# Kernel optimization log

Measured on AMD Instinct MI355X. Metric: run time of the kernel, lower is better.

Reference implementation:

```python
import jax, jax.numpy as jnp
import numpy as np

INP = 1024          # inp_size
N = 8000            # n_neurons
NE = 6400           # n_e_neurons = 0.8*N
NI = 1600           # n_i_neurons = 0.2*N
TS = 1000           # ts_sim = t_sim/dt = 1.0/0.001
PRB0, PRB1 = 200, 1000  # probe window in timesteps
DT = 0.001
TAU = 0.02
VTH = 0.5
RATE = 0.5          # rate_scale
NORM = float(PRB1 - PRB0)  # spike_p_norm


def setup_inputs() -> dict:
    key = jax.random.key(0)
    k1, k2, k3, k4, k5, k6 = jax.random.split(key, 6)
    inp = jax.random.uniform(k1, (INP,), dtype=jnp.float32)
    A = INP + N
    # Sparse random recurrent weights, faithful in structure to init_w:
    # rows [0:INP+NE] carry excitatory (positive) weights, last NI rows inhibitory (negative).
    sign = jnp.concatenate([jnp.ones(INP + NE, jnp.float32), -jnp.ones(NI, jnp.float32)])[:, None]
    mask_e = (jax.random.uniform(k2, (A, NE)) < 0.05).astype(jnp.float32)
    w_ae = sign * mask_e * jax.random.uniform(k3, (A, NE), dtype=jnp.float32) * 0.1
    mask_i = (jax.random.uniform(k4, (A, NI)) < 0.05).astype(jnp.float32)
    w_ai = sign * mask_i * jax.random.uniform(k5, (A, NI), dtype=jnp.float32) * 0.1
    # Precomputed per-timestep uniform noise (replaces torch.rand_like in the loop)
    rand_p = jax.random.uniform(k6, (TS, INP), dtype=jnp.float32)
    return {"inp": inp, "w_ae": w_ae, "w_ai": w_ai, "rand_p": rand_p}


def reference(inp, w_ae, w_ai, rand_p):
    inp_s = inp * RATE
    decay = 1.0 - DT / TAU  # vmem += -vmem/tau*dt  ==  vmem *= (1 - dt/tau)

    def step(carry, r):
        vmem, sl, slp = carry  # spike_l, spike_l_prev as float32 {0,1}
        sp = (r <= inp_s).astype(jnp.float32)  # Poisson input spikes
        v = vmem * decay
        # excitatory targets see prev-step E spikes + current I spikes; inhibitory the reverse
        in_e = jnp.concatenate([sp, slp[:NE], sl[NE:]])   # [INP+N]
        in_i = jnp.concatenate([sp, sl[:NE], slp[NE:]])   # [INP+N]
        v = v + jnp.concatenate([in_e @ w_ae, in_i @ w_ai])  # [N]
        new_sl = (v >= VTH).astype(jnp.float32)
        v = v * (1.0 - new_sl)  # reset fired neurons to 0
        return (v, new_sl, sl), new_sl[:NE]

    init = (jnp.zeros(N, jnp.float32), jnp.zeros(N, jnp.float32), jnp.zeros(N, jnp.float32))
    _, e_spikes = jax.lax.scan(step, init, rand_p)  # [TS, NE]
    sumspike_e = e_spikes[PRB0:PRB1].sum(axis=0)
    return sumspike_e / NORM
```

## Files before the change

### kernel.cpp

```cpp
#include <hip/hip_runtime.h>
#include <stdint.h>

#define INP_N   1024
#define NE_N    6400
#define NI_N    1600
#define NCOL    8000
#define TS_N    1000
#define PRB0_T  200
#define TSPLIT  16
#define NCHUNK  12
#define CAPTOT  992
#define IN_ENT  112
#define BC      64
#define NWV     8
#define CAPE    24
#define NBLD    (125 * 12)

enum : size_t {
  ROWS_OFF = 0,
  VALS_OFF = ROWS_OFF + (size_t)CAPTOT * NCOL * 2,
  CNT_OFF  = VALS_OFF + (size_t)CAPTOT * NCOL * 4,
  CSUM_OFF = CNT_OFF  + (size_t)NCHUNK * NCOL * 4,
  DRV_OFF  = CSUM_OFF + (size_t)NCHUNK * NCOL * 4,
  SE_OFF   = DRV_OFF  + (size_t)TS_N * NCOL * 4,
  SI_OFF   = SE_OFF   + (size_t)NCOL * 4,
  FLG_OFF  = SI_OFF   + (size_t)NCOL * 4,
  STV_OFF  = FLG_OFF  + (size_t)TS_N * 4,
  STR_OFF  = STV_OFF  + (size_t)8192 * 4,
  STT_OFF  = STR_OFF  + (size_t)512 * 8,
  SAB_OFF  = STT_OFF  + (size_t)8 * 4,
  AFL_OFF  = SAB_OFF  + 4,
  MNP_OFF  = AFL_OFF  + 4,
  MNW_OFF  = MNP_OFF  + 32 * 4,
  STG_OFF  = MNW_OFF  + 64 * 4,
  OVA_OFF  = STG_OFF  + 4,
  CTR_OFF  = OVA_OFF  + (size_t)NBLD * 4,
};

__device__ __forceinline__ void chunk_info(int c, int& j0, int& len, int& cap, int& off) {
  if (c < 2) { j0 = c * 512;            len = 512; cap = 56; off = c * 56; }
  else       { j0 = 1024 + (c - 2) * 800; len = 800; cap = 88; off = 112 + (c - 2) * 88; }
}

__global__ void __launch_bounds__(512) k_build(
    const float* __restrict__ w_ae, const float* __restrict__ w_ai,
    uint16_t* __restrict__ rows, float* __restrict__ vals,
    int* __restrict__ cnt, float* __restrict__ csum, int* __restrict__ ovfA,
    float* __restrict__ gv, unsigned long long* __restrict__ gring,
    int* __restrict__ gtot, unsigned int* __restrict__ ctr) {
  __shared__ uint16_t rs_s[NWV * CAPE * BC];
  __shared__ float    vs_s[NWV * CAPE * BC];
  __shared__ int      kqs[NWV][BC];
  __shared__ float    sqs[NWV][BC];
  __shared__ int      wovf[NWV];
  const int tid   = threadIdx.x;
  const int lane  = tid & 63;
  const int wv    = tid >> 6;
  const int chunk = blockIdx.y;
  const int col0  = blockIdx.x * BC;

  if (blockIdx.x == 0 && blockIdx.y == 0) {
    for (int i = tid; i < 8192; i += 512) gv[i] = 0.f;
    if (tid < 512) gring[tid] = (tid < 512) ? 0ull : 0ull;
    if (tid < 8) gtot[tid] = 0;
    if (tid < 2) ctr[tid] = 0u;
  }

  int j0, len, cap, off;
  chunk_info(chunk, j0, len, cap, off);
  const float* W; int nc, cc0;
  if (col0 < NE_N) { W = w_ae; nc = NE_N; cc0 = col0; }
  else             { W = w_ai; nc = NI_N; cc0 = col0 - NE_N; }

  const int qlen = len >> 3;
  const int j0w  = j0 + wv * qlen;
  const float* Wc = W + (size_t)j0w * nc + cc0 + lane;

  float cur[16], nxt[16];
  #pragma unroll
  for (int r = 0; r < 16; ++r) cur[r] = Wc[(size_t)r * nc];

  int k = 0; float s = 0.f; int ovfl = 0;
  for (int t0 = 0; t0 < qlen; t0 += 16) {
    const int nt = t0 + 16;
    if (nt < qlen) {
      #pragma unroll
      for (int r = 0; r < 16; ++r) {
        int rq = nt + r; rq = rq < qlen ? rq : qlen - 1;
        nxt[r] = Wc[(size_t)rq * nc];
      }
    }
    const int rlim = (qlen - t0) < 16 ? (qlen - t0) : 16;
    #pragma unroll
    for (int r = 0; r < 16; ++r) {
      if (r < rlim) {
        float w = cur[r];
        if (w != 0.f) {
          if (k < CAPE) {
            rs_s[(wv * CAPE + k) * BC + lane] = (uint16_t)(j0w + t0 + r);
            vs_s[(wv * CAPE + k) * BC + lane] = w;
            s += w; ++k;
          } else ovfl = 1;
        }
      }
    }
    #pragma unroll
    for (int r = 0; r < 16; ++r) cur[r] = nxt[r];
  }
  kqs[wv][lane] = k;
  sqs[wv][lane] = s;
  int anyo = __any(ovfl);
  if (lane == 0) wovf[wv] = anyo;
  __syncthreads();

  const int col = lane;
  int c[NWV + 1]; c[0] = 0;
  #pragma unroll
  for (int q = 0; q < NWV; ++q) c[q + 1] = c[q] + kqs[q][col];
  const int ktot = c[NWV];
  if (tid < BC) {
    cnt[chunk * NCOL + col0 + col] = ktot < cap ? ktot : cap;
    float ss = sqs[0][col];
    #pragma unroll
    for (int q = 1; q < NWV; ++q) ss += sqs[q][col];
    csum[chunk * NCOL + col0 + col] = ss;
    unsigned long long capov = __ballot(ktot > cap);
    if (tid == 0) {
      int o = capov ? 1 : 0;
      #pragma unroll
      for (int q = 0; q < NWV; ++q) o |= wovf[q];
      ovfA[blockIdx.y * gridDim.x + blockIdx.x] = o;
    }
  }
  const int wlim = (chunk < 2) ? cap : (ktot < cap ? ktot : cap);
  const size_t gb = (size_t)off * NCOL + col0;
  for (int kk = wv; kk < wlim; kk += NWV) {
    uint16_t rr = (uint16_t)j0; float vv = 0.f;
    if (kk < ktot) {
      int q = 0;
      #pragma unroll
      for (int qq = 1; qq < NWV; ++qq) if (kk >= c[qq]) q = qq;
      int loc = kk - c[q];
      rr = rs_s[(q * CAPE + loc) * BC + col];
      vv = vs_s[(q * CAPE + loc) * BC + col];
    }
    rows[gb + (size_t)kk * NCOL + col] = rr;
    vals[gb + (size_t)kk * NCOL + col] = vv;
  }
}

__global__ void __launch_bounds__(256) k_proof(
    const float* __restrict__ csum, float* __restrict__ sE, float* __restrict__ sI,
    const float* __restrict__ vals, float* __restrict__ minpart, float* __restrict__ mwpart,
    const int* __restrict__ ovfA, unsigned int* __restrict__ ctr, int* __restrict__ strongp) {
  const int tid = threadIdx.x;
  const int b = blockIdx.x;
  __shared__ float w4[4];
  __shared__ int lastS;
  float m = 1e30f;
  if (b < 32) {
    int col = b * 256 + tid;
    if (col < NCOL) {
      float se = 0.f;
      #pragma unroll
      for (int c = 2; c <= 9; ++c) se += csum[c * NCOL + col];
      float si = csum[10 * NCOL + col] + csum[11 * NCOL + col];
      sE[col] = se;
      sI[col] = si;
      m = se + si;
    }
  } else {
    const int n = IN_ENT * NCOL;
    for (int i = (b - 32) * 256 + tid; i < n; i += 64 * 256)
      m = fminf(m, vals[i]);
  }
  #pragma unroll
  for (int o = 32; o; o >>= 1) m = fminf(m, __shfl_down(m, o));
  if ((tid & 63) == 0) w4[tid >> 6] = m;
  __syncthreads();
  if (tid == 0) {
    float r = fminf(fminf(w4[0], w4[1]), fminf(w4[2], w4[3]));
    if (b < 32) minpart[b] = r; else mwpart[b - 32] = r;
    __threadfence();
    unsigned p = __hip_atomic_fetch_add(&ctr[0], 1u, __ATOMIC_ACQ_REL, __HIP_MEMORY_SCOPE_AGENT);
    lastS = (p == 95) ? 1 : 0;
  }
  __syncthreads();
  if (!lastS) return;
  __threadfence();
  float mb = (tid < 32) ? __hip_atomic_load(&minpart[tid], __ATOMIC_RELAXED, __HIP_MEMORY_SCOPE_AGENT) : 1e30f;
  float mw = (tid < 64) ? __hip_atomic_load(&mwpart[tid],  __ATOMIC_RELAXED, __HIP_MEMORY_SCOPE_AGENT) : 1e30f;
  int ov = 0;
  for (int i = tid; i < NBLD; i += 256)
    ov |= __hip_atomic_load(&ovfA[i], __ATOMIC_RELAXED, __HIP_MEMORY_SCOPE_AGENT);
  #pragma unroll
  for (int o = 32; o; o >>= 1) {
    mb = fminf(mb, __shfl_down(mb, o));
    mw = fminf(mw, __shfl_down(mw, o));
    ov |= __shfl_down(ov, o);
  }
  __shared__ float fm[4], fw[4]; __shared__ int fo[4];
  if ((tid & 63) == 0) { fm[tid >> 6] = mb; fw[tid >> 6] = mw; fo[tid >> 6] = ov; }
  __syncthreads();
  if (tid == 0) {
    float MB = fminf(fminf(fm[0], fm[1]), fminf(fm[2], fm[3]));
    float MW = fminf(fminf(fw[0], fw[1]), fminf(fw[2], fw[3]));
    int   OV = fo[0] | fo[1] | fo[2] | fo[3];
    strongp[0] = (MB >= 1.0f && MW >= 0.0f && OV == 0) ? 1 : 0;
  }
}

__global__ void __launch_bounds__(256) k_drive(
    const uint16_t* __restrict__ rows, const float* __restrict__ vals,
    const float* __restrict__ rand_p, const float* __restrict__ inp,
    float* __restrict__ drive,
    const int* __restrict__ strongp, const int* __restrict__ sabp, int pass) {
  int t0, t1;
  if (pass == 0) {
    if (strongp[0]) {
      if (blockIdx.y >= 4) return;
      t0 = blockIdx.y * 4; t1 = t0 + 4;
    } else { t0 = blockIdx.y * 40; t1 = t0 + 40; }
  } else {
    if (!strongp[0] || sabp[0]) return;
    t0 = blockIdx.y * 40; t1 = t0 + 40;
    if (blockIdx.y == 0) t0 = TSPLIT;
  }
  __shared__ uint16_t rs[IN_ENT * 64];
  __shared__ float    vs[IN_ENT * 64];
  __shared__ float    inps[INP_N];
  __shared__ float    act0[INP_N];
  __shared__ float    psum[4][64];
  const int tid = threadIdx.x, lane = tid & 63, ph = tid >> 6;
  const int col0 = blockIdx.x * 64;
  for (int idx = tid; idx < IN_ENT * 64; idx += 256) {
    int k = idx >> 6, l = idx & 63;
    rs[idx] = rows[(size_t)k * NCOL + col0 + l];
    vs[idx] = vals[(size_t)k * NCOL + col0 + l];
  }
  for (int i = tid; i < INP_N; i += 256) inps[i] = inp[i] * 0.5f;
  __syncthreads();
  for (int t = t0; t < t1; ++t) {
    #pragma unroll
    for (int i = tid; i < INP_N; i += 256)
      act0[i] = (rand_p[(size_t)t * INP_N + i] <= inps[i]) ? 1.f : 0.f;
    __syncthreads();
    float acc = 0.f;
    for (int k = ph; k < IN_ENT; k += 4)
      acc += vs[k * 64 + lane] * act0[rs[k * 64 + lane]];
    psum[ph][lane] = acc;
    __syncthreads();
    if (ph == 0)
      drive[(size_t)t * NCOL + col0 + lane] =
        ((psum[0][lane] + psum[1][lane]) + psum[2][lane]) + psum[3][lane];
    __syncthreads();
  }
}

__global__ void __launch_bounds__(1024) k_step(
    const uint16_t* __restrict__ rows, const float* __restrict__ vals,
    const int* __restrict__ cnt, const float* __restrict__ sE,
    const float* __restrict__ sI, const float* __restrict__ drive,
    float* __restrict__ gv, unsigned long long* __restrict__ gring,
    int* __restrict__ gtot, const int* __restrict__ strongp, int t) {
  __shared__ unsigned long long m[128];
  __shared__ float psum[16][64];
  const int tid = threadIdx.x, lane = tid & 63, ph = tid >> 6;
  const int blk = blockIdx.x;
  const bool isE = (blk < 100);
  const int sw = t & 3, s1 = (t + 3) & 3, s2 = (t + 2) & 3;

  const bool full1 = (gtot[s1] == NE_N) && (gtot[4 + s1] == NI_N);
  const bool full2 = (gtot[s2] == NE_N) && (gtot[4 + s2] == NI_N);
  if (strongp[0] && full1 && full2) {
    if (tid == 0) {
      gring[sw * 128 + blk] = ~0ull;
      if (blk == 0) { gtot[sw] = NE_N; gtot[4 + sw] = NI_N; }
    }
    return;
  }

  const int sEs = isE ? s2 : s1;
  const int sIs = isE ? s1 : s2;
  const int col = blk * 64 + lane;

  if (tid < 100)      m[tid] = gring[sEs * 128 + tid];
  else if (tid < 125) m[tid] = gring[sIs * 128 + tid];
  const int pEv = gtot[sEs];
  const int pIv = gtot[4 + sIs];
  if (blk == 0 && tid == 0) { gtot[(t + 1) & 3] = 0; gtot[4 + ((t + 1) & 3)] = 0; }
  __syncthreads();

  float acc = 0.f;
  if (pEv > 0 && pEv < NE_N) {
    for (int c = 2; c <= 9; ++c) {
      int cn = cnt[c * NCOL + col];
      size_t base = (size_t)(112 + (c - 2) * 88) * NCOL + col;
      for (int k = ph; k < cn; k += 16) {
        int r = rows[base + (size_t)k * NCOL] - 1024;
        float wv = vals[base + (size_t)k * NCOL];
        if ((m[r >> 6] >> (r & 63)) & 1ull) acc += wv;
      }
    }
  }
  if (pIv > 0 && pIv < NI_N) {
    for (int c = 10; c <= 11; ++c) {
      int cn = cnt[c * NCOL + col];
      size_t base = (size_t)(112 + (c - 2) * 88) * NCOL + col;
      for (int k = ph; k < cn; k += 16) {
        int r = rows[base + (size_t)k * NCOL] - 1024;
        float wv = vals[base + (size_t)k * NCOL];
        if ((m[r >> 6] >> (r & 63)) & 1ull) acc += wv;
      }
    }
  }
  psum[ph][lane] = acc;
  __syncthreads();

  if (ph == 0) {
    float ps = 0.f;
    #pragma unroll
    for (int q = 0; q < 16; ++q) ps += psum[q][lane];
    float tot = drive[(size_t)t * NCOL + col] + ps;
    if (pEv == NE_N) tot += sE[col];
    if (pIv == NI_N) tot += sI[col];
    float vn = gv[col] * 0.95f + tot;
    int s = (vn >= 0.5f) ? 1 : 0;
    gv[col] = s ? 0.f : vn;
    unsigned long long bal = __ballot(s);
    int pc = __popcll(bal);
    if (lane == 0) {
      gring[sw * 128 + blk] = bal;
      if (isE) atomicAdd(&gtot[sw], pc);
      else     atomicAdd(&gtot[4 + sw], pc);
    }
  }
}

__global__ void __launch_bounds__(512) k_tail(
    const uint16_t* __restrict__ rows, const float* __restrict__ vals,
    const int* __restrict__ cnt, const float* __restrict__ sE,
    const float* __restrict__ sI, const float* __restrict__ drive,
    float* __restrict__ gv, unsigned long long* __restrict__ gring,
    int* __restrict__ gtot, const int* __restrict__ strongp,
    unsigned int* __restrict__ ctr) {
  __shared__ unsigned long long m[128];
  __shared__ float psum[8][64];
  const int tid = threadIdx.x, lane = tid & 63, ph = tid >> 6;
  const int blk = blockIdx.x;
  const bool isE = (blk < 100);

  const bool full8 = (gtot[0] == NE_N) && (gtot[4] == NI_N);
  const bool full9 = (gtot[1] == NE_N) && (gtot[5] == NI_N);
  if (strongp[0] && full8 && full9) {
    if (blk == 0) {
      for (int i = tid; i < 512; i += 512) gring[i] = ~0ull;
      if (tid < 4) { gtot[tid] = NE_N; gtot[4 + tid] = NI_N; }
    }
    return;
  }

  for (int t = 10; t < 16; ++t) {
    const int sw = t & 3, s1 = (t + 3) & 3, s2 = (t + 2) & 3;
    const int sEs = isE ? s2 : s1, sIs = isE ? s1 : s2;
    if (tid < 100)
      m[tid] = __hip_atomic_load(&gring[sEs * 128 + tid], __ATOMIC_RELAXED, __HIP_MEMORY_SCOPE_AGENT);
    else if (tid < 125)
      m[tid] = __hip_atomic_load(&gring[sIs * 128 + tid], __ATOMIC_RELAXED, __HIP_MEMORY_SCOPE_AGENT);
    const int pEv = __hip_atomic_load(&gtot[sEs], __ATOMIC_RELAXED, __HIP_MEMORY_SCOPE_AGENT);
    const int pIv = __hip_atomic_load(&gtot[4 + sIs], __ATOMIC_RELAXED, __HIP_MEMORY_SCOPE_AGENT);
    if (blk == 0 && tid == 0) {
      __hip_atomic_store(&gtot[(t + 1) & 3], 0, __ATOMIC_RELAXED, __HIP_MEMORY_SCOPE_AGENT);
      __hip_atomic_store(&gtot[4 + ((t + 1) & 3)], 0, __ATOMIC_RELAXED, __HIP_MEMORY_SCOPE_AGENT);
    }
    __syncthreads();

    const int col = blk * 64 + lane;
    float acc = 0.f;
    if (pEv > 0 && pEv < NE_N) {
      for (int c = 2; c <= 9; ++c) {
        int cn = cnt[c * NCOL + col];
        size_t base = (size_t)(112 + (c - 2) * 88) * NCOL + col;
        for (int k = ph; k < cn; k += 8) {
          int r = rows[base + (size_t)k * NCOL] - 1024;
          float wv = vals[base + (size_t)k * NCOL];
          if ((m[r >> 6] >> (r & 63)) & 1ull) acc += wv;
        }
      }
    }
    if (pIv > 0 && pIv < NI_N) {
      for (int c = 10; c <= 11; ++c) {
        int cn = cnt[c * NCOL + col];
        size_t base = (size_t)(112 + (c - 2) * 88) * NCOL + col;
        for (int k = ph; k < cn; k += 8) {
          int r = rows[base + (size_t)k * NCOL] - 1024;
          float wv = vals[base + (size_t)k * NCOL];
          if ((m[r >> 6] >> (r & 63)) & 1ull) acc += wv;
        }
      }
    }
    psum[ph][lane] = acc;
    __syncthreads();

    if (ph == 0) {
      float tot = drive[(size_t)t * NCOL + col]
                + ((psum[0][lane] + psum[1][lane]) + (psum[2][lane] + psum[3][lane]))
                + ((psum[4][lane] + psum[5][lane]) + (psum[6][lane] + psum[7][lane]));
      if (pEv == NE_N) tot += sE[col];
      if (pIv == NI_N) tot += sI[col];
      float vn = gv[col] * 0.95f + tot;
      int s = (vn >= 0.5f) ? 1 : 0;
      gv[col] = s ? 0.f : vn;
      unsigned long long bal = __ballot(s);
      int pc = __popcll(bal);
      if (lane == 0) {
        __hip_atomic_store(&gring[sw * 128 + blk], bal, __ATOMIC_RELAXED, __HIP_MEMORY_SCOPE_AGENT);
        if (isE) atomicAdd(&gtot[sw], pc);
        else     atomicAdd(&gtot[4 + sw], pc);
      }
    }
    __syncthreads();
    if (tid == 0) {
      __threadfence();
      __hip_atomic_fetch_add(&ctr[1], 1u, __ATOMIC_RELEASE, __HIP_MEMORY_SCOPE_AGENT);
      const unsigned tgt = (unsigned)(t - 9) * 125;
      while (__hip_atomic_load(&ctr[1], __ATOMIC_ACQUIRE, __HIP_MEMORY_SCOPE_AGENT) < tgt)
        __builtin_amdgcn_s_sleep(1);
    }
    __syncthreads();
  }
}

__global__ void k_sab(const int* __restrict__ gtot, int* __restrict__ sab) {
  sab[0] = (gtot[1] == NE_N && gtot[2] == NE_N && gtot[3] == NE_N &&
            gtot[5] == NI_N && gtot[6] == NI_N && gtot[7] == NI_N) ? 1 : 0;
}

__global__ void __launch_bounds__(256) k_check2(
    const float* __restrict__ drive, const float* __restrict__ sE,
    const float* __restrict__ sI, int* __restrict__ flag,
    const int* __restrict__ strongp, const int* __restrict__ sabp) {
  if (strongp[0] && sabp[0]) return;
  const int tid = threadIdx.x;
  __shared__ int w4[4];
  for (int t = blockIdx.x; t < TS_N; t += 125) {
    const float* dr = drive + (size_t)t * NCOL;
    int nb = 0;
    for (int col = tid; col < NCOL; col += 256) {
      float vn = (dr[col] + sE[col]) + sI[col];
      nb += (vn >= 0.5f) ? 0 : 1;
    }
    #pragma unroll
    for (int o = 32; o; o >>= 1) nb += __shfl_down(nb, o);
    if ((tid & 63) == 0) w4[tid >> 6] = nb;
    __syncthreads();
    if (tid == 0) flag[t] = ((w4[0] + w4[1]) + (w4[2] + w4[3])) == 0 ? 1 : 0;
    __syncthreads();
  }
}

__global__ void k_fin(const int* __restrict__ flag, const int* __restrict__ strongp,
                      int* __restrict__ allflag) {
  const int tid = threadIdx.x;
  if (strongp[0]) { if (tid == 0) allflag[0] = 1; return; }
  int bad = 0;
  for (int i = TSPLIT + tid; i < TS_N; i += 256) bad += (flag[i] == 0) ? 1 : 0;
  #pragma unroll
  for (int o = 32; o; o >>= 1) bad += __shfl_down(bad, o);
  __shared__ int w4[4];
  if ((tid & 63) == 0) w4[tid >> 6] = bad;
  __syncthreads();
  if (tid == 0) allflag[0] = ((w4[0] + w4[1]) + (w4[2] + w4[3])) == 0 ? 1 : 0;
}

__global__ void __launch_bounds__(1024) k_simB(
    const uint16_t* __restrict__ rows, const float* __restrict__ vals,
    const int* __restrict__ cnt, const float* __restrict__ sE,
    const float* __restrict__ sI, const float* __restrict__ drive,
    const int* __restrict__ flag,
    const float* __restrict__ stv, const unsigned long long* __restrict__ str_,
    const int* __restrict__ stt, const int* __restrict__ sab,
    const int* __restrict__ allflag, float* __restrict__ out) {
  __shared__ unsigned long long ring[4][128];
  __shared__ int pEtot[4], pItot[4];
  __shared__ int flagsL[TS_N];
  __shared__ int fastexit;

  const int tid  = threadIdx.x;
  const int lane = tid & 63;
  const int wv   = tid >> 6;

  if (tid == 0) fastexit = (sab[0] != 0) && (allflag[0] != 0);
  __syncthreads();

  if (fastexit) {
    #pragma unroll
    for (int p = 0; p < 8; ++p) {
      int col = p * 1024 + tid;
      if (col < NE_N) out[col] = 1.0f;
    }
    return;
  }

  for (int i = tid; i < 512; i += 1024) (&ring[0][0])[i] = str_[i];
  if (tid < 4) { pEtot[tid] = stt[tid]; pItot[tid] = stt[4 + tid]; }
  for (int i = tid; i < TS_N; i += 1024) flagsL[i] = flag[i];

  float v[8], sEr[8], sIr[8];
  int spk[8];
  #pragma unroll
  for (int p = 0; p < 8; ++p) {
    int col = p * 1024 + tid;
    sEr[p] = (col < NCOL) ? sE[col] : 0.f;
    sIr[p] = (col < NCOL) ? sI[col] : 0.f;
    v[p] = (col < NCOL) ? stv[col] : 0.f; spk[p] = 0;
  }
  int spkAll = 0, fastAge = 0;
  __syncthreads();

  for (int t = TSPLIT; t < TS_N; ++t) {
    const int sw = t & 3, s1 = (t + 3) & 3, s2 = (t + 2) & 3;
    int pE1, pI1, pE2, pI2;
    if (fastAge >= 2)      { pE1 = pE2 = NE_N; pI1 = pI2 = NI_N; }
    else if (fastAge == 1) { pE1 = NE_N; pI1 = NI_N; pE2 = pEtot[s2]; pI2 = pItot[s2]; }
    else                   { pE1 = pEtot[s1]; pI1 = pItot[s1]; pE2 = pEtot[s2]; pI2 = pItot[s2]; }
    const bool satE1 = (pE1 == NE_N), satE2 = (pE2 == NE_N);
    const bool satI1 = (pI1 == NI_N), satI2 = (pI2 == NI_N);

    if (satE1 && satI1 && satE2 && satI2 && flagsL[t]) {
      if (t >= PRB0_T) ++spkAll;
      ++fastAge;
      continue;
    }

    if (fastAge > 0) {
      for (int i = tid; i < 128; i += 1024) {
        ring[s1][i] = ~0ull;
        if (fastAge >= 2) ring[s2][i] = ~0ull;
      }
    }
    if (tid == 0) {
      if (fastAge > 0) {
        pEtot[s1] = NE_N; pItot[s1] = NI_N;
        if (fastAge >= 2) { pEtot[s2] = NE_N; pItot[s2] = NI_N; }
      }
      pEtot[sw] = 0; pItot[sw] = 0;
    }
    __syncthreads();
    fastAge = 0;

    const float* dr = drive + (size_t)t * NCOL;
    int myE = 0, myI = 0;
    #pragma unroll
    for (int p = 0; p < 8; ++p) {
      int col = p * 1024 + tid;
      bool isEcol = col < NE_N;
      int pEv = isEcol ? pE2 : pE1;
      int pIv = isEcol ? pI1 : pI2;
      int sEs = isEcol ? s2 : s1;
      int sIs = isEcol ? s1 : s2;
      float tot = (col < NCOL) ? dr[col] : 0.f;
      if (col < NCOL) {
        if (pEv == NE_N) tot += sEr[p];
        else if (pEv > 0) {
          for (int c = 2; c <= 9; ++c) {
            int cn = cnt[c * NCOL + col];
            size_t base = (size_t)(112 + (c - 2) * 88) * NCOL + col;
            for (int k = 0; k < cn; ++k) {
              int j = rows[base + (size_t)k * NCOL];
              float wval = vals[base + (size_t)k * NCOL];
              int r = j - 1024;
              if ((ring[sEs][r >> 6] >> (r & 63)) & 1ull) tot += wval;
            }
          }
        }
        if (pIv == NI_N) tot += sIr[p];
        else if (pIv > 0) {
          for (int c = 10; c <= 11; ++c) {
            int cn = cnt[c * NCOL + col];
            size_t base = (size_t)(112 + (c - 2) * 88) * NCOL + col;
            for (int k = 0; k < cn; ++k) {
              int j = rows[base + (size_t)k * NCOL];
              float wval = vals[base + (size_t)k * NCOL];
              int r = j - 1024;
              if ((ring[sIs][r >> 6] >> (r & 63)) & 1ull) tot += wval;
            }
          }
        }
      }
      float vn = v[p] * 0.95f + tot;
      int s = (col < NCOL) && (vn >= 0.5f);
      v[p] = s ? 0.f : vn;
      if (t >= PRB0_T && isEcol) spk[p] += s;
      unsigned long long bal = __ballot(s);
      int word = p * 16 + wv;
      if (word < 125) {
        int pc = __popcll(bal);
        if (word < 100) myE += pc; else myI += pc;
        if (lane == 0) ring[sw][word] = bal;
      }
    }
    if (lane == 0) { atomicAdd(&pEtot[sw], myE); atomicAdd(&pItot[sw], myI); }
    __syncthreads();
  }

  #pragma unroll
  for (int p = 0; p < 8; ++p) {
    int col = p * 1024 + tid;
    if (col < NE_N) out[col] = (float)(spk[p] + spkAll) / 800.0f;
  }
}

extern "C" void kernel_launch(void* const* d_in, const int* in_sizes, int n_in,
                              void* d_out, int out_size, void* d_ws, size_t ws_size,
                              hipStream_t stream) {
  const float* inp    = (const float*)d_in[0];
  const float* w_ae   = (const float*)d_in[1];
  const float* w_ai   = (const float*)d_in[2];
  const float* rand_p = (const float*)d_in[3];

  char* ws = (char*)d_ws;
  uint16_t*           rows    = (uint16_t*)(ws + ROWS_OFF);
  float*              vals    = (float*)(ws + VALS_OFF);
  int*                cnt     = (int*)(ws + CNT_OFF);
  float*              csum    = (float*)(ws + CSUM_OFF);
  float*              drive   = (float*)(ws + DRV_OFF);
  float*              sEa     = (float*)(ws + SE_OFF);
  float*              sIa     = (float*)(ws + SI_OFF);
  int*                flag    = (int*)(ws + FLG_OFF);
  float*              gv      = (float*)(ws + STV_OFF);
  unsigned long long* gring   = (unsigned long long*)(ws + STR_OFF);
  int*                gtot    = (int*)(ws + STT_OFF);
  int*                sab     = (int*)(ws + SAB_OFF);
  int*                afl     = (int*)(ws + AFL_OFF);
  float*              minpart = (float*)(ws + MNP_OFF);
  float*              mwpart  = (float*)(ws + MNW_OFF);
  int*                strg    = (int*)(ws + STG_OFF);
  int*                ovfA    = (int*)(ws + OVA_OFF);
  unsigned int*       ctr     = (unsigned int*)(ws + CTR_OFF);

  k_build<<<dim3(NCOL / BC, NCHUNK), 512, 0, stream>>>(w_ae, w_ai, rows, vals, cnt, csum,
                                                       ovfA, gv, gring, gtot, ctr);
  k_proof<<<96, 256, 0, stream>>>(csum, sEa, sIa, vals, minpart, mwpart, ovfA, ctr, strg);
  k_drive<<<dim3(125, 25), 256, 0, stream>>>(rows, vals, rand_p, inp, drive, strg, sab, 0);
  for (int t = 0; t < 10; ++t)
    k_step<<<125, 1024, 0, stream>>>(rows, vals, cnt, sEa, sIa, drive, gv, gring, gtot, strg, t);
  k_tail<<<125, 512, 0, stream>>>(rows, vals, cnt, sEa, sIa, drive, gv, gring, gtot, strg, ctr);
  k_sab<<<1, 1, 0, stream>>>(gtot, sab);
  k_drive<<<dim3(125, 25), 256, 0, stream>>>(rows, vals, rand_p, inp, drive, strg, sab, 1);
  k_check2<<<125, 256, 0, stream>>>(drive, sEa, sIa, flag, strg, sab);
  k_fin<<<1, 256, 0, stream>>>(flag, strg, afl);
  k_simB<<<1, 1024, 0, stream>>>(rows, vals, cnt, sEa, sIa, drive, flag,
                                 gv, gring, gtot, sab, afl, (float*)d_out);
}
```

Baseline: 534.0 us.

## Fuse first sixteen timesteps and input drive into one persistent kernel

Replaces the ten per-timestep k_step launches, k_tail and k_sab with a single persistent kernel that simulates steps 0-15. It uses a grid-wide counter barrier between steps, computes the Poisson input drive for those steps in shared memory, and sets the saturation flag itself. The aim is to remove about a dozen kernel launches and the global drive round-trip for the early steps. In exchange, steps 0-9 now run on 512-thread blocks instead of 1024 and pay spin-barrier costs. The early-exit path also now returns out of the whole loop.

```diff
diff --git a/kernel.cpp b/kernel.cpp
--- a/kernel.cpp
+++ b/kernel.cpp
@@ -61,7 +61,7 @@
 
   if (blockIdx.x == 0 && blockIdx.y == 0) {
     for (int i = tid; i < 8192; i += 512) gv[i] = 0.f;
-    if (tid < 512) gring[tid] = (tid < 512) ? 0ull : 0ull;
+    gring[tid] = 0ull;
     if (tid < 8) gtot[tid] = 0;
     if (tid < 2) ctr[tid] = 0u;
   }
@@ -217,10 +217,8 @@
     const int* __restrict__ strongp, const int* __restrict__ sabp, int pass) {
   int t0, t1;
   if (pass == 0) {
-    if (strongp[0]) {
-      if (blockIdx.y >= 4) return;
-      t0 = blockIdx.y * 4; t1 = t0 + 4;
-    } else { t0 = blockIdx.y * 40; t1 = t0 + 40; }
+    if (strongp[0]) return;
+    t0 = blockIdx.y * 40; t1 = t0 + 40;
   } else {
     if (!strongp[0] || sabp[0]) return;
     t0 = blockIdx.y * 40; t1 = t0 + 40;
@@ -257,125 +255,84 @@
   }
 }
 
-__global__ void __launch_bounds__(1024) k_step(
+__global__ void __launch_bounds__(512) k_sim16(
     const uint16_t* __restrict__ rows, const float* __restrict__ vals,
     const int* __restrict__ cnt, const float* __restrict__ sE,
-    const float* __restrict__ sI, const float* __restrict__ drive,
+    const float* __restrict__ sI, const float* __restrict__ rand_p,
+    const float* __restrict__ inp,
     float* __restrict__ gv, unsigned long long* __restrict__ gring,
-    int* __restrict__ gtot, const int* __restrict__ strongp, int t) {
+    int* __restrict__ gtot, const int* __restrict__ strongp,
+    unsigned int* __restrict__ ctr, int* __restrict__ sab) {
+  __shared__ uint16_t rs[IN_ENT * 64];
+  __shared__ float    vs[IN_ENT * 64];
+  __shared__ float    inps[INP_N];
+  __shared__ float    act0[INP_N];
+  __shared__ float    drv[16][64];
   __shared__ unsigned long long m[128];
-  __shared__ float psum[16][64];
+  __shared__ float    psum[8][64];
   const int tid = threadIdx.x, lane = tid & 63, ph = tid >> 6;
   const int blk = blockIdx.x;
   const bool isE = (blk < 100);
-  const int sw = t & 3, s1 = (t + 3) & 3, s2 = (t + 2) & 3;
-
-  const bool full1 = (gtot[s1] == NE_N) && (gtot[4 + s1] == NI_N);
-  const bool full2 = (gtot[s2] == NE_N) && (gtot[4 + s2] == NI_N);
-  if (strongp[0] && full1 && full2) {
-    if (tid == 0) {
-      gring[sw * 128 + blk] = ~0ull;
-      if (blk == 0) { gtot[sw] = NE_N; gtot[4 + sw] = NI_N; }
-    }
-    return;
-  }
-
-  const int sEs = isE ? s2 : s1;
-  const int sIs = isE ? s1 : s2;
-  const int col = blk * 64 + lane;
-
-  if (tid < 100)      m[tid] = gring[sEs * 128 + tid];
-  else if (tid < 125) m[tid] = gring[sIs * 128 + tid];
-  const int pEv = gtot[sEs];
-  const int pIv = gtot[4 + sIs];
-  if (blk == 0 && tid == 0) { gtot[(t + 1) & 3] = 0; gtot[4 + ((t + 1) & 3)] = 0; }
-  __syncthreads();
-
-  float acc = 0.f;
-  if (pEv > 0 && pEv < NE_N) {
-    for (int c = 2; c <= 9; ++c) {
-      int cn = cnt[c * NCOL + col];
-      size_t base = (size_t)(112 + (c - 2) * 88) * NCOL + col;
-      for (int k = ph; k < cn; k += 16) {
-        int r = rows[base + (size_t)k * NCOL] - 1024;
-        float wv = vals[base + (size_t)k * NCOL];
-        if ((m[r >> 6] >> (r & 63)) & 1ull) acc += wv;
-      }
-    }
-  }
-  if (pIv > 0 && pIv < NI_N) {
-    for (int c = 10; c <= 11; ++c) {
-      int cn = cnt[c * NCOL + col];
-      size_t base = (size_t)(112 + (c - 2) * 88) * NCOL + col;
-      for (int k = ph; k < cn; k += 16) {
-        int r = rows[base + (size_t)k * NCOL] - 1024;
-        float wv = vals[base + (size_t)k * NCOL];
-        if ((m[r >> 6] >> (r & 63)) & 1ull) acc += wv;
-      }
-    }
-  }
-  psum[ph][lane] = acc;
-  __syncthreads();
-
-  if (ph == 0) {
-    float ps = 0.f;
-    #pragma unroll
-    for (int q = 0; q < 16; ++q) ps += psum[q][lane];
-    float tot = drive[(size_t)t * NCOL + col] + ps;
-    if (pEv == NE_N) tot += sE[col];
-    if (pIv == NI_N) tot += sI[col];
-    float vn = gv[col] * 0.95f + tot;
-    int s = (vn >= 0.5f) ? 1 : 0;
-    gv[col] = s ? 0.f : vn;
-    unsigned long long bal = __ballot(s);
-    int pc = __popcll(bal);
-    if (lane == 0) {
-      gring[sw * 128 + blk] = bal;
-      if (isE) atomicAdd(&gtot[sw], pc);
-      else     atomicAdd(&gtot[4 + sw], pc);
-    }
-  }
-}
-
-__global__ void __launch_bounds__(512) k_tail(
-    const uint16_t* __restrict__ rows, const float* __restrict__ vals,
-    const int* __restrict__ cnt, const float* __restrict__ sE,
-    const float* __restrict__ sI, const float* __restrict__ drive,
-    float* __restrict__ gv, unsigned long long* __restrict__ gring,
-    int* __restrict__ gtot, const int* __restrict__ strongp,
-    unsigned int* __restrict__ ctr) {
-  __shared__ unsigned long long m[128];
-  __shared__ float psum[8][64];
-  const int tid = threadIdx.x, lane = tid & 63, ph = tid >> 6;
-  const int blk = blockIdx.x;
-  const bool isE = (blk < 100);
-
-  const bool full8 = (gtot[0] == NE_N) && (gtot[4] == NI_N);
-  const bool full9 = (gtot[1] == NE_N) && (gtot[5] == NI_N);
-  if (strongp[0] && full8 && full9) {
-    if (blk == 0) {
-      for (int i = tid; i < 512; i += 512) gring[i] = ~0ull;
-      if (tid < 4) { gtot[tid] = NE_N; gtot[4 + tid] = NI_N; }
-    }
-    return;
-  }
-
-  for (int t = 10; t < 16; ++t) {
+  const int col0 = blk * 64, col = col0 + lane;
+  const int strong = strongp[0];
+
+  for (int idx = tid; idx < IN_ENT * 64; idx += 512) {
+    int k = idx >> 6, l = idx & 63;
+    rs[idx] = rows[(size_t)k * NCOL + col0 + l];
+    vs[idx] = vals[(size_t)k * NCOL + col0 + l];
+  }
+  for (int i = tid; i < INP_N; i += 512) inps[i] = inp[i] * 0.5f;
+  __syncthreads();
+
+  for (int t = 0; t < 16; ++t) {
+    for (int i = tid; i < INP_N; i += 512)
+      act0[i] = (rand_p[(size_t)t * INP_N + i] <= inps[i]) ? 1.f : 0.f;
+    __syncthreads();
+    float acc = 0.f;
+    for (int k = ph; k < IN_ENT; k += 8)
+      acc += vs[k * 64 + lane] * act0[rs[k * 64 + lane]];
+    psum[ph][lane] = acc;
+    __syncthreads();
+    if (ph == 0)
+      drv[t][lane] = ((psum[0][lane] + psum[1][lane]) + (psum[2][lane] + psum[3][lane]))
+                   + ((psum[4][lane] + psum[5][lane]) + (psum[6][lane] + psum[7][lane]));
+    __syncthreads();
+  }
+
+  for (int t = 0; t < 16; ++t) {
     const int sw = t & 3, s1 = (t + 3) & 3, s2 = (t + 2) & 3;
-    const int sEs = isE ? s2 : s1, sIs = isE ? s1 : s2;
+    const int pE1 = __hip_atomic_load(&gtot[s1], __ATOMIC_RELAXED, __HIP_MEMORY_SCOPE_AGENT);
+    const int pI1 = __hip_atomic_load(&gtot[4 + s1], __ATOMIC_RELAXED, __HIP_MEMORY_SCOPE_AGENT);
+    const int pE2 = __hip_atomic_load(&gtot[s2], __ATOMIC_RELAXED, __HIP_MEMORY_SCOPE_AGENT);
+    const int pI2 = __hip_atomic_load(&gtot[4 + s2], __ATOMIC_RELAXED, __HIP_MEMORY_SCOPE_AGENT);
+    const bool full1 = (pE1 == NE_N) && (pI1 == NI_N);
+    const bool full2 = (pE2 == NE_N) && (pI2 == NI_N);
+
+    if (strong && full1 && full2) {
+      if (blk == 0 && tid == 0) {
+        for (int q = 0; q < 4; ++q) {
+          __hip_atomic_store(&gtot[q], NE_N, __ATOMIC_RELAXED, __HIP_MEMORY_SCOPE_AGENT);
+          __hip_atomic_store(&gtot[4 + q], NI_N, __ATOMIC_RELAXED, __HIP_MEMORY_SCOPE_AGENT);
+        }
+        __hip_atomic_store(sab, 1, __ATOMIC_RELEASE, __HIP_MEMORY_SCOPE_AGENT);
+      }
+      return;
+    }
+
+    const int sEs = isE ? s2 : s1;
+    const int sIs = isE ? s1 : s2;
     if (tid < 100)
       m[tid] = __hip_atomic_load(&gring[sEs * 128 + tid], __ATOMIC_RELAXED, __HIP_MEMORY_SCOPE_AGENT);
     else if (tid < 125)
       m[tid] = __hip_atomic_load(&gring[sIs * 128 + tid], __ATOMIC_RELAXED, __HIP_MEMORY_SCOPE_AGENT);
-    const int pEv = __hip_atomic_load(&gtot[sEs], __ATOMIC_RELAXED, __HIP_MEMORY_SCOPE_AGENT);
-    const int pIv = __hip_atomic_load(&gtot[4 + sIs], __ATOMIC_RELAXED, __HIP_MEMORY_SCOPE_AGENT);
+    const int pEv = isE ? pE2 : pE1;
+    const int pIv = isE ? pI1 : pI2;
     if (blk == 0 && tid == 0) {
       __hip_atomic_store(&gtot[(t + 1) & 3], 0, __ATOMIC_RELAXED, __HIP_MEMORY_SCOPE_AGENT);
       __hip_atomic_store(&gtot[4 + ((t + 1) & 3)], 0, __ATOMIC_RELAXED, __HIP_MEMORY_SCOPE_AGENT);
     }
     __syncthreads();
 
-    const int col = blk * 64 + lane;
     float acc = 0.f;
     if (pEv > 0 && pEv < NE_N) {
       for (int c = 2; c <= 9; ++c) {
@@ -403,7 +360,7 @@
     __syncthreads();
 
     if (ph == 0) {
-      float tot = drive[(size_t)t * NCOL + col]
+      float tot = drv[t][lane]
                 + ((psum[0][lane] + psum[1][lane]) + (psum[2][lane] + psum[3][lane]))
                 + ((psum[4][lane] + psum[5][lane]) + (psum[6][lane] + psum[7][lane]));
       if (pEv == NE_N) tot += sE[col];
@@ -423,17 +380,22 @@
     if (tid == 0) {
       __threadfence();
       __hip_atomic_fetch_add(&ctr[1], 1u, __ATOMIC_RELEASE, __HIP_MEMORY_SCOPE_AGENT);
-      const unsigned tgt = (unsigned)(t - 9) * 125;
+      const unsigned tgt = (unsigned)(t + 1) * 125;
       while (__hip_atomic_load(&ctr[1], __ATOMIC_ACQUIRE, __HIP_MEMORY_SCOPE_AGENT) < tgt)
         __builtin_amdgcn_s_sleep(1);
     }
     __syncthreads();
   }
-}
-
-__global__ void k_sab(const int* __restrict__ gtot, int* __restrict__ sab) {
-  sab[0] = (gtot[1] == NE_N && gtot[2] == NE_N && gtot[3] == NE_N &&
-            gtot[5] == NI_N && gtot[6] == NI_N && gtot[7] == NI_N) ? 1 : 0;
+
+  if (blk == 0 && tid == 0) {
+    int ok = (__hip_atomic_load(&gtot[1], __ATOMIC_RELAXED, __HIP_MEMORY_SCOPE_AGENT) == NE_N &&
+              __hip_atomic_load(&gtot[2], __ATOMIC_RELAXED, __HIP_MEMORY_SCOPE_AGENT) == NE_N &&
+              __hip_atomic_load(&gtot[3], __ATOMIC_RELAXED, __HIP_MEMORY_SCOPE_AGENT) == NE_N &&
+              __hip_atomic_load(&gtot[5], __ATOMIC_RELAXED, __HIP_MEMORY_SCOPE_AGENT) == NI_N &&
+              __hip_atomic_load(&gtot[6], __ATOMIC_RELAXED, __HIP_MEMORY_SCOPE_AGENT) == NI_N &&
+              __hip_atomic_load(&gtot[7], __ATOMIC_RELAXED, __HIP_MEMORY_SCOPE_AGENT) == NI_N) ? 1 : 0;
+    __hip_atomic_store(sab, ok, __ATOMIC_RELEASE, __HIP_MEMORY_SCOPE_AGENT);
+  }
 }
 
 __global__ void __launch_bounds__(256) k_check2(
@@ -643,10 +605,8 @@
                                                        ovfA, gv, gring, gtot, ctr);
   k_proof<<<96, 256, 0, stream>>>(csum, sEa, sIa, vals, minpart, mwpart, ovfA, ctr, strg);
   k_drive<<<dim3(125, 25), 256, 0, stream>>>(rows, vals, rand_p, inp, drive, strg, sab, 0);
-  for (int t = 0; t < 10; ++t)
-    k_step<<<125, 1024, 0, stream>>>(rows, vals, cnt, sEa, sIa, drive, gv, gring, gtot, strg, t);
-  k_tail<<<125, 512, 0, stream>>>(rows, vals, cnt, sEa, sIa, drive, gv, gring, gtot, strg, ctr);
-  k_sab<<<1, 1, 0, stream>>>(gtot, sab);
+  k_sim16<<<125, 512, 0, stream>>>(rows, vals, cnt, sEa, sIa, rand_p, inp,
+                                   gv, gring, gtot, strg, ctr, sab);
   k_drive<<<dim3(125, 25), 256, 0, stream>>>(rows, vals, rand_p, inp, drive, strg, sab, 1);
   k_check2<<<125, 256, 0, stream>>>(drive, sEa, sIa, flag, strg, sab);
   k_fin<<<1, 256, 0, stream>>>(flag, strg, afl);
```

Result: slower. 739.0 us (+38.4%).
